# Kernel tuning notes

Hardware: AMD Instinct MI355X
Metric: run time of the kernel (lower is better)

## Reference

```python
import jax, jax.numpy as jnp
import numpy as np

B, BOND, N, ATOM, UNITS = 256, 5, 128, 64, 128


def setup_inputs() -> dict:
    key = jax.random.key(0)
    k1, k2, k3 = jax.random.split(key, 3)
    adjacency = jax.random.uniform(k1, (B, BOND, N, N), dtype=jnp.float32)
    features = jax.random.normal(k2, (B, N, ATOM), dtype=jnp.float32)
    # per-sample unique kernel: (global_batch, bond_dim, atom_dim, units)
    kernel = jax.random.normal(k3, (B, BOND, ATOM, UNITS), dtype=jnp.float32) * 0.05
    return {"adjacency": adjacency, "features": features, "kernel": kernel}


def reference(adjacency, features, kernel):
    # aggregate neighbors per bond type: [B, bond, N, atom]
    x = jnp.einsum('bemn,bnd->bemd', adjacency, features)
    # per-sample, per-bond linear transform: [B, bond, N, units]
    x = jnp.einsum('bemd,bedu->bemu', x, kernel)
    # reduce over bond types, then activation: [B, N, units]
    return jax.nn.relu(jnp.sum(x, axis=1))
```

## Files before the change

kernel.cpp:

```cpp
#include <hip/hip_runtime.h>


typedef __attribute__((ext_vector_type(8))) short s8v;
typedef __attribute__((ext_vector_type(4))) short s4v;
typedef __attribute__((ext_vector_type(4))) float f4v;

__device__ __forceinline__ short f2bf(float f) {
    unsigned u = __builtin_bit_cast(unsigned, f);
    u += 0x7FFFu + ((u >> 16) & 1u);
    return (short)(u >> 16);
}

__device__ __forceinline__ void lds_barrier() {
    asm volatile("s_waitcnt lgkmcnt(0)" ::: "memory");
    __builtin_amdgcn_s_barrier();
    __builtin_amdgcn_sched_barrier(0);
}

__global__ __launch_bounds__(1024, 4)
void rgc_kernel(const float* __restrict__ adj,
                const float* __restrict__ feat,
                const float* __restrict__ ker,
                float* __restrict__ out)
{
    __shared__ __align__(16) short featA[16 * 512];
    __shared__ __align__(16) short kerB[5][16 * 512];
    __shared__ __align__(16) short WB[2][32 * 512];

    const int tid  = threadIdx.x;
    const int w    = tid >> 6;
    const int lane = tid & 63;
    const int c16  = lane & 15;
    const int quad = lane >> 4;
    const int g    = w >> 1;
    const int h    = w & 1;

    const int b = blockIdx.x;
    const float* adjB = adj  + (size_t)b * (5 * 128 * 128);
    const float* feG  = feat + (size_t)b * (128 * 64);
    const float* keG  = ker  + (size_t)b * (5 * 64 * 128);
    float*       outB = out  + (size_t)b * (128 * 128);

    f4v a0[4], a1[4];
    {
        const float* ap = adjB + (16 * g + c16) * 128 + 8 * quad;
        #pragma unroll
        for (int k16 = 0; k16 < 4; ++k16) {
            a0[k16] = *(const f4v*)(ap + 32 * k16);
            a1[k16] = *(const f4v*)(ap + 32 * k16 + 4);
        }
    }

    {
        const float* fp = feG + (16 * (w >> 1) + c16) * 64 + 32 * (w & 1) + 8 * quad;
        f4v f0 = *(const f4v*)(fp);
        f4v f1 = *(const f4v*)(fp + 4);
        s8v v;
        #pragma unroll
        for (int j = 0; j < 4; ++j) { v[j] = f2bf(f0[j]); v[4 + j] = f2bf(f1[j]); }
        *(s8v*)&featA[w * 512 + lane * 8] = v;
    }

    const int ku  = tid & 127;
    const int kd0 = (tid >> 7) * 8;
    const int kerB_off = (ku >> 4) * 1024 + (kd0 >> 5) * 512 + ((kd0 >> 3) & 3) * 128 + (ku & 15) * 8;
    {
        float kv[5][8];
        #pragma unroll
        for (int e = 0; e < 5; ++e)
            #pragma unroll
            for (int j = 0; j < 8; ++j)
                kv[e][j] = keG[e * (64 * 128) + (kd0 + j) * 128 + ku];
        #pragma unroll
        for (int e = 0; e < 5; ++e) {
            s8v v;
            #pragma unroll
            for (int j = 0; j < 8; ++j) v[j] = f2bf(kv[e][j]);
            *(s8v*)&kerB[e][kerB_off] = v;
        }
    }
    lds_barrier();

    const int wk16 = g >> 1;
    const int wqt  = 2 * (g & 1) + (quad >> 1);
    const int wj0  = 4 * (quad & 1);
    const int wbase = (wqt * 16 + c16) * 8 + wj0;

    {
        s8v fa0 = *(const s8v*)&featA[(g * 2 + 0) * 512 + lane * 8];
        s8v fa1 = *(const s8v*)&featA[(g * 2 + 1) * 512 + lane * 8];
        #pragma unroll
        for (int t = 0; t < 4; ++t) {
            const int u16 = 4 * h + t;
            s8v kb0 = *(const s8v*)&kerB[0][(u16 * 2 + 0) * 512 + lane * 8];
            s8v kb1 = *(const s8v*)&kerB[0][(u16 * 2 + 1) * 512 + lane * 8];
            f4v wacc = {};
            wacc = __builtin_amdgcn_mfma_f32_16x16x32_bf16(fa0, kb0, wacc, 0, 0, 0);
            wacc = __builtin_amdgcn_mfma_f32_16x16x32_bf16(fa1, kb1, wacc, 0, 0, 0);
            s4v pv;
            #pragma unroll
            for (int r = 0; r < 4; ++r) pv[r] = f2bf(wacc[r]);
            *(s4v*)&WB[0][(u16 * 4 + wk16) * 512 + wbase] = pv;
        }
    }
    lds_barrier();

    f4v oacc[4] = {};

    for (int e = 0; e < 5; ++e) {
        s8v af[4];
        #pragma unroll
        for (int k16 = 0; k16 < 4; ++k16) {
            #pragma unroll
            for (int j = 0; j < 4; ++j) {
                af[k16][j]     = f2bf(a0[k16][j]);
                af[k16][4 + j] = f2bf(a1[k16][j]);
            }
        }

        if (e < 4) {
            const float* ap = adjB + (e + 1) * (128 * 128) + (16 * g + c16) * 128 + 8 * quad;
            #pragma unroll
            for (int k16 = 0; k16 < 4; ++k16) {
                a0[k16] = *(const f4v*)(ap + 32 * k16);
                a1[k16] = *(const f4v*)(ap + 32 * k16 + 4);
            }
            __builtin_amdgcn_sched_barrier(0);

            s8v fa0 = *(const s8v*)&featA[(g * 2 + 0) * 512 + lane * 8];
            s8v fa1 = *(const s8v*)&featA[(g * 2 + 1) * 512 + lane * 8];
            #pragma unroll
            for (int t = 0; t < 4; ++t) {
                const int u16 = 4 * h + t;
                s8v kb0 = *(const s8v*)&kerB[e + 1][(u16 * 2 + 0) * 512 + lane * 8];
                s8v kb1 = *(const s8v*)&kerB[e + 1][(u16 * 2 + 1) * 512 + lane * 8];
                f4v wacc = {};
                wacc = __builtin_amdgcn_mfma_f32_16x16x32_bf16(fa0, kb0, wacc, 0, 0, 0);
                wacc = __builtin_amdgcn_mfma_f32_16x16x32_bf16(fa1, kb1, wacc, 0, 0, 0);
                s4v pv;
                #pragma unroll
                for (int r = 0; r < 4; ++r) pv[r] = f2bf(wacc[r]);
                *(s4v*)&WB[(e + 1) & 1][(u16 * 4 + wk16) * 512 + wbase] = pv;
            }
        }

        #pragma unroll
        for (int n = 0; n < 4; ++n) {
            const int u16 = 4 * h + n;
            #pragma unroll
            for (int k16 = 0; k16 < 4; ++k16) {
                s8v bfr = *(const s8v*)&WB[e & 1][(u16 * 4 + k16) * 512 + lane * 8];
                oacc[n] = __builtin_amdgcn_mfma_f32_16x16x32_bf16(af[k16], bfr, oacc[n], 0, 0, 0);
            }
        }

        if (e < 4) lds_barrier();
    }

    #pragma unroll
    for (int n = 0; n < 4; ++n)
        #pragma unroll
        for (int r = 0; r < 4; ++r)
            outB[(16 * g + 4 * quad + r) * 128 + 16 * (4 * h + n) + c16] = fmaxf(oacc[n][r], 0.f);
}

extern "C" void kernel_launch(void* const* d_in, const int* in_sizes, int n_in,
                              void* d_out, int out_size, void* d_ws, size_t ws_size,
                              hipStream_t stream)
{
    const float* adj  = (const float*)d_in[0];
    const float* feat = (const float*)d_in[1];
    const float* ker  = (const float*)d_in[2];
    rgc_kernel<<<256, 1024, 0, stream>>>(adj, feat, ker, (float*)d_out);
}
```

Baseline: 170.2 us.

## Split fused kernel into W-precompute and output kernels via workspace

Splits the single fused kernel (256 blocks of 1024 threads) into two launches. The first computes W = features·kernel per (sample, bond) in bf16 into the workspace using 1280 blocks. The second computes the adjacency·W products over 16-row slices using 2048 smaller blocks with a swizzled block order. The aim is more parallelism and better GPU occupancy than one block per sample. In exchange it adds a second launch and a workspace round trip through global memory, and it falls back to the old kernel if the workspace is too small.

```diff
diff --git a/kernel.cpp b/kernel.cpp
--- a/kernel.cpp
+++ b/kernel.cpp
@@ -15,6 +15,146 @@
     asm volatile("s_waitcnt lgkmcnt(0)" ::: "memory");
     __builtin_amdgcn_s_barrier();
     __builtin_amdgcn_sched_barrier(0);
+}
+
+__global__ __launch_bounds__(256, 4)
+void w_kernel(const float* __restrict__ feat,
+              const float* __restrict__ ker,
+              short* __restrict__ wsF)
+{
+    __shared__ __align__(16) short kerF[16 * 512];
+
+    const int bid  = blockIdx.x;
+    const int b    = bid / 5;
+    const int tid  = threadIdx.x;
+    const int w    = tid >> 6;
+    const int lane = tid & 63;
+    const int c16  = lane & 15;
+    const int qd   = lane >> 4;
+
+    const float* keG  = ker  + (size_t)bid * (64 * 128);
+    const float* feB  = feat + (size_t)b * (128 * 64);
+    short*       wOut = wsF  + (size_t)bid * 16384;
+
+    {
+        const int d  = tid >> 2;
+        const int u0 = (tid & 3) * 32;
+        const float* kp = keG + d * 128 + u0;
+        f4v kv[8];
+        #pragma unroll
+        for (int i = 0; i < 8; ++i) kv[i] = *(const f4v*)(kp + 4 * i);
+        const int kk = d >> 5, q = (d >> 3) & 3, j = d & 7;
+        #pragma unroll
+        for (int i = 0; i < 8; ++i)
+            #pragma unroll
+            for (int c = 0; c < 4; ++c) {
+                const int u = u0 + 4 * i + c;
+                kerF[((u >> 4) * 2 + kk) * 512 + (q * 16 + (u & 15)) * 8 + j] = f2bf(kv[i][c]);
+            }
+    }
+    __syncthreads();
+
+    #pragma unroll
+    for (int n16 = 0; n16 < 8; ++n16) {
+        const float* fp = feB + (16 * n16 + c16) * 64 + 8 * qd;
+        f4v f00 = *(const f4v*)(fp);
+        f4v f01 = *(const f4v*)(fp + 4);
+        f4v f10 = *(const f4v*)(fp + 32);
+        f4v f11 = *(const f4v*)(fp + 36);
+        s8v fa0, fa1;
+        #pragma unroll
+        for (int j = 0; j < 4; ++j) {
+            fa0[j] = f2bf(f00[j]); fa0[4 + j] = f2bf(f01[j]);
+            fa1[j] = f2bf(f10[j]); fa1[4 + j] = f2bf(f11[j]);
+        }
+        #pragma unroll
+        for (int t = 0; t < 2; ++t) {
+            const int u16 = 2 * w + t;
+            s8v kb0 = *(const s8v*)&kerF[(u16 * 2 + 0) * 512 + lane * 8];
+            s8v kb1 = *(const s8v*)&kerF[(u16 * 2 + 1) * 512 + lane * 8];
+            f4v wacc = {};
+            wacc = __builtin_amdgcn_mfma_f32_16x16x32_bf16(fa0, kb0, wacc, 0, 0, 0);
+            wacc = __builtin_amdgcn_mfma_f32_16x16x32_bf16(fa1, kb1, wacc, 0, 0, 0);
+            s4v pv;
+            #pragma unroll
+            for (int r = 0; r < 4; ++r) pv[r] = f2bf(wacc[r]);
+            *(s4v*)(wOut + (u16 * 4 + (n16 >> 1)) * 512
+                         + ((2 * (n16 & 1) + (qd >> 1)) * 16 + c16) * 8
+                         + 4 * (qd & 1)) = pv;
+        }
+    }
+}
+
+__global__ __launch_bounds__(256, 4)
+void out_kernel(const float* __restrict__ adj,
+                const short* __restrict__ wsF,
+                float* __restrict__ out)
+{
+    const int bid = blockIdx.x;
+    const int wg  = ((bid & 7) << 8) | (bid >> 3);
+    const int b   = wg >> 3;
+    const int R0  = 16 * (wg & 7);
+    const int tid  = threadIdx.x;
+    const int w    = tid >> 6;
+    const int lane = tid & 63;
+    const int c16  = lane & 15;
+    const int qd   = lane >> 4;
+
+    const float* adjB = adj + (size_t)b * (5 * 128 * 128);
+    const short* wB   = wsF + (size_t)b * 5 * 16384;
+    float*       outB = out + (size_t)b * (128 * 128);
+
+    f4v a0[4], a1[4];
+    {
+        const float* ap = adjB + (R0 + c16) * 128 + 8 * qd;
+        #pragma unroll
+        for (int k = 0; k < 4; ++k) {
+            a0[k] = *(const f4v*)(ap + 32 * k);
+            a1[k] = *(const f4v*)(ap + 32 * k + 4);
+        }
+    }
+
+    f4v oacc[2] = {};
+
+    for (int e = 0; e < 5; ++e) {
+        s8v af[4];
+        #pragma unroll
+        for (int k = 0; k < 4; ++k)
+            #pragma unroll
+            for (int j = 0; j < 4; ++j) {
+                af[k][j]     = f2bf(a0[k][j]);
+                af[k][4 + j] = f2bf(a1[k][j]);
+            }
+
+        s8v wv[8];
+        #pragma unroll
+        for (int t = 0; t < 2; ++t)
+            #pragma unroll
+            for (int k = 0; k < 4; ++k)
+                wv[t * 4 + k] = *(const s8v*)&wB[e * 16384 + ((2 * w + t) * 4 + k) * 512 + lane * 8];
+
+        if (e < 4) {
+            const float* ap = adjB + (e + 1) * 16384 + (R0 + c16) * 128 + 8 * qd;
+            #pragma unroll
+            for (int k = 0; k < 4; ++k) {
+                a0[k] = *(const f4v*)(ap + 32 * k);
+                a1[k] = *(const f4v*)(ap + 32 * k + 4);
+            }
+            __builtin_amdgcn_sched_barrier(0);
+        }
+
+        #pragma unroll
+        for (int t = 0; t < 2; ++t)
+            #pragma unroll
+            for (int k = 0; k < 4; ++k)
+                oacc[t] = __builtin_amdgcn_mfma_f32_16x16x32_bf16(af[k], wv[t * 4 + k], oacc[t], 0, 0, 0);
+    }
+
+    #pragma unroll
+    for (int t = 0; t < 2; ++t)
+        #pragma unroll
+        for (int r = 0; r < 4; ++r)
+            outB[(R0 + 4 * qd + r) * 128 + 16 * (2 * w + t) + c16] = fmaxf(oacc[t][r], 0.f);
 }
 
 __global__ __launch_bounds__(1024, 4)
@@ -50,7 +190,6 @@
             a1[k16] = *(const f4v*)(ap + 32 * k16 + 4);
         }
     }
-
     {
         const float* fp = feG + (16 * (w >> 1) + c16) * 64 + 32 * (w & 1) + 8 * quad;
         f4v f0 = *(const f4v*)(fp);
@@ -60,7 +199,6 @@
         for (int j = 0; j < 4; ++j) { v[j] = f2bf(f0[j]); v[4 + j] = f2bf(f1[j]); }
         *(s8v*)&featA[w * 512 + lane * 8] = v;
     }
-
     const int ku  = tid & 127;
     const int kd0 = (tid >> 7) * 8;
     const int kerB_off = (ku >> 4) * 1024 + (kd0 >> 5) * 512 + ((kd0 >> 3) & 3) * 128 + (ku & 15) * 8;
@@ -106,7 +244,6 @@
     lds_barrier();
 
     f4v oacc[4] = {};
-
     for (int e = 0; e < 5; ++e) {
         s8v af[4];
         #pragma unroll
@@ -117,7 +254,6 @@
                 af[k16][4 + j] = f2bf(a1[k16][j]);
             }
         }
-
         if (e < 4) {
             const float* ap = adjB + (e + 1) * (128 * 128) + (16 * g + c16) * 128 + 8 * quad;
             #pragma unroll
@@ -143,7 +279,6 @@
                 *(s4v*)&WB[(e + 1) & 1][(u16 * 4 + wk16) * 512 + wbase] = pv;
             }
         }
-
         #pragma unroll
         for (int n = 0; n < 4; ++n) {
             const int u16 = 4 * h + n;
@@ -153,7 +288,6 @@
                 oacc[n] = __builtin_amdgcn_mfma_f32_16x16x32_bf16(af[k16], bfr, oacc[n], 0, 0, 0);
             }
         }
-
         if (e < 4) lds_barrier();
     }
 
@@ -171,5 +305,11 @@
     const float* adj  = (const float*)d_in[0];
     const float* feat = (const float*)d_in[1];
     const float* ker  = (const float*)d_in[2];
-    rgc_kernel<<<256, 1024, 0, stream>>>(adj, feat, ker, (float*)d_out);
-}
+    const size_t W_BYTES = (size_t)1280 * 16384 * sizeof(short);
+    if (ws_size >= W_BYTES) {
+        w_kernel<<<1280, 256, 0, stream>>>(feat, ker, (short*)d_ws);
+        out_kernel<<<2048, 256, 0, stream>>>(adj, (const short*)d_ws, (float*)d_out);
+    } else {
+        rgc_kernel<<<256, 1024, 0, stream>>>(adj, feat, ker, (float*)d_out);
+    }
+}
```

Result: slower. 215.2 us (+26.4%).
